# Kernel optimization log

Hardware: AMD Instinct MI355X
Metric: run time of the kernel (lower is better)

The kernel has to match this reference:

```python
import jax, jax.numpy as jnp
import numpy as np

B, N, P, D = 32, 128, 8, 512


def setup_inputs() -> dict:
    key = jax.random.key(0)
    k_x, k_w1, k_b1, k_w2, k_b2 = jax.random.split(key, 5)
    lim = 1.0 / np.sqrt(D)  # torch Linear init range
    x = jax.random.normal(k_x, (B, N, P, D), dtype=jnp.float32)
    # torch Linear weights are [out, in]; stack per-patch -> [P, D, D]
    W1 = jax.random.uniform(k_w1, (P, D, D), minval=-lim, maxval=lim, dtype=jnp.float32)
    b1 = jax.random.uniform(k_b1, (P, D), minval=-lim, maxval=lim, dtype=jnp.float32)
    W2 = jax.random.uniform(k_w2, (P, D, D), minval=-lim, maxval=lim, dtype=jnp.float32)
    b2 = jax.random.uniform(k_b2, (P, D), minval=-lim, maxval=lim, dtype=jnp.float32)
    return {"x": x, "W1": W1, "b1": b1, "W2": W2, "b2": b2}


def reference(x, W1, b1, W2, b2):
    # Per-patch 2-layer MLP with GELU, batched as one grouped GEMM pair.
    # torch Linear: y = x @ W.T + b  ->  einsum over 'kd' with W[p, k, d]
    h = jnp.einsum('bnpd,pkd->bnpk', x, W1) + b1  # [B, N, P, D]
    h = jax.nn.gelu(h, approximate=False)          # nn.GELU default is exact
    o = jnp.einsum('bnpd,pkd->bnpk', h, W2) + b2  # [B, N, P, D]
    # Dropout p=0.0 -> identity. Residual add.
    return o + x
```

## Files before the change

kernel.cpp:

```cpp
#include <hip/hip_runtime.h>
#include <stdint.h>


typedef unsigned short u16;
typedef __attribute__((ext_vector_type(8))) short bf16x8;
typedef __attribute__((ext_vector_type(4))) float f32x4;

#define AS1 __attribute__((address_space(1)))
#define AS3 __attribute__((address_space(3)))

#define MTOT 4096
#define PATCHES 8
#define DDIM 512
#define ROWSTRIDE 4096

__device__ __forceinline__ void glds16(const void* g, void* l) {
  __builtin_amdgcn_global_load_lds((const AS1 uint32_t*)g, (AS3 uint32_t*)l, 16, 0, 0);
}

__device__ __forceinline__ u16 bf16_rne(float v) {
  union { float f; uint32_t u; } c; c.f = v;
  uint32_t u = c.u + 0x7FFFu + ((c.u >> 16) & 1u);
  return (u16)(u >> 16);
}
__device__ __forceinline__ float bf16_to_f(u16 h) {
  union { uint32_t u; float f; } c; c.u = ((uint32_t)h) << 16;
  return c.f;
}
__device__ __forceinline__ void split2(float v, u16& hi, u16& lo) {
  hi = bf16_rne(v);
  float r = v - bf16_to_f(hi);
  lo = bf16_rne(r);
}

__global__ void split3_kernel(const float* __restrict__ x,  u16* xhi,  u16* xlo,  int nx,
                              const float* __restrict__ w1, u16* w1hi, u16* w1lo,
                              const float* __restrict__ w2, u16* w2hi, u16* w2lo, int nw) {
  const int total4 = (nx + 2 * nw) >> 2;
  for (int i4 = blockIdx.x * blockDim.x + threadIdx.x; i4 < total4;
       i4 += gridDim.x * blockDim.x) {
    int i = i4 << 2;
    const float* src; u16* h; u16* l; int off;
    if (i < nx)           { src = x;  h = xhi;  l = xlo;  off = i; }
    else if (i < nx + nw) { src = w1; h = w1hi; l = w1lo; off = i - nx; }
    else                  { src = w2; h = w2hi; l = w2lo; off = i - nx - nw; }
    float4 v = *reinterpret_cast<const float4*>(src + off);
    ushort4 hh, ll;
    split2(v.x, hh.x, ll.x);
    split2(v.y, hh.y, ll.y);
    split2(v.z, hh.z, ll.z);
    split2(v.w, hh.w, ll.w);
    *reinterpret_cast<ushort4*>(h + off) = hh;
    *reinterpret_cast<ushort4*>(l + off) = ll;
  }
}

template <int EPI>
__global__ __launch_bounds__(512, 2) void gemm_split8(
    const u16* __restrict__ Ahi, const u16* __restrict__ Alo,
    const u16* __restrict__ Bhi, const u16* __restrict__ Blo,
    const float* __restrict__ bias,
    const float* __restrict__ resid,
    u16* __restrict__ OutHi, u16* __restrict__ OutLo,
    float* __restrict__ OutF)
{
  const int nwg = gridDim.x;
  const int bid = blockIdx.x;
  const int swz = (bid & 7) * (nwg >> 3) + (bid >> 3);
  const int nt = swz & 1;
  const int mt = (swz >> 1) & 15;
  const int p  = swz >> 5;

  __shared__ __attribute__((aligned(16))) u16 sm[2][4][256 * 32];

  const int t    = threadIdx.x;
  const int lane = t & 63;
  const int wv   = t >> 6;
  const int wr   = wv >> 2;
  const int wc   = wv & 3;
  const int fr   = lane & 15;
  const int cS   = (lane >> 4) ^ ((fr >> 1) & 3);

  const int sr0 = t >> 2;
  const int sc  = t & 3;
  const int scS = sc ^ ((sr0 >> 1) & 3);
  const int se0 = t * 8;
  const int se1 = se0 + 4096;

  const size_t aG0 = (size_t)(mt * 256 + sr0)       * ROWSTRIDE + (size_t)p * DDIM + scS * 8;
  const size_t aG1 = (size_t)(mt * 256 + sr0 + 128) * ROWSTRIDE + (size_t)p * DDIM + scS * 8;
  const size_t bG0 = ((size_t)p * DDIM + nt * 256 + sr0)       * DDIM + scS * 8;
  const size_t bG1 = ((size_t)p * DDIM + nt * 256 + sr0 + 128) * DDIM + scS * 8;

  f32x4 acc[8][4] = {};

  glds16(Ahi + aG0, &sm[0][0][se0]); glds16(Ahi + aG1, &sm[0][0][se1]);
  glds16(Alo + aG0, &sm[0][1][se0]); glds16(Alo + aG1, &sm[0][1][se1]);
  glds16(Bhi + bG0, &sm[0][2][se0]); glds16(Bhi + bG1, &sm[0][2][se1]);
  glds16(Blo + bG0, &sm[0][3][se0]); glds16(Blo + bG1, &sm[0][3][se1]);
  asm volatile("s_waitcnt vmcnt(0)" ::: "memory");
  __builtin_amdgcn_s_barrier();

#define DS_A(pl, m) (*(const bf16x8*)&sm[cur][pl][(wr * 128 + (m) * 16 + fr) * 32 + cS * 8])
#define DS_B(pl, n) (*(const bf16x8*)&sm[cur][pl][(wc * 64  + (n) * 16 + fr) * 32 + cS * 8])
#define MFMA3(m, a_h, a_l)                                                            \
  _Pragma("unroll")                                                                   \
  for (int n = 0; n < 4; ++n) {                                                       \
    acc[m][n] = __builtin_amdgcn_mfma_f32_16x16x32_bf16(a_h, bh[n], acc[m][n], 0,0,0);\
    acc[m][n] = __builtin_amdgcn_mfma_f32_16x16x32_bf16(a_l, bh[n], acc[m][n], 0,0,0);\
    acc[m][n] = __builtin_amdgcn_mfma_f32_16x16x32_bf16(a_h, bl[n], acc[m][n], 0,0,0);\
  }

  for (int kt = 0; kt < 16; ++kt) {
    const int cur = kt & 1, nxt = cur ^ 1;
    const bool stage = (kt != 15);
    const size_t ko = (size_t)(kt + 1) * 32;

    bf16x8 bh[4], bl[4];

    {
#pragma unroll
      for (int n = 0; n < 4; ++n) { bh[n] = DS_B(2, n); bl[n] = DS_B(3, n); }
      bf16x8 a0h = DS_A(0, 0), a1h = DS_A(0, 1);
      bf16x8 a0l = DS_A(1, 0), a1l = DS_A(1, 1);
      if (stage) { glds16(Ahi + aG0 + ko, &sm[nxt][0][se0]);
                   glds16(Ahi + aG1 + ko, &sm[nxt][0][se1]); }
      __builtin_amdgcn_s_barrier();
      asm volatile("s_waitcnt lgkmcnt(0)" ::: "memory");
      __builtin_amdgcn_s_setprio(1);
      MFMA3(0, a0h, a0l)
      MFMA3(1, a1h, a1l)
      __builtin_amdgcn_s_setprio(0);
      __builtin_amdgcn_s_barrier();
    }
    {
      bf16x8 a0h = DS_A(0, 2), a1h = DS_A(0, 3);
      bf16x8 a0l = DS_A(1, 2), a1l = DS_A(1, 3);
      if (stage) { glds16(Alo + aG0 + ko, &sm[nxt][1][se0]);
                   glds16(Alo + aG1 + ko, &sm[nxt][1][se1]); }
      __builtin_amdgcn_s_barrier();
      asm volatile("s_waitcnt lgkmcnt(0)" ::: "memory");
      __builtin_amdgcn_s_setprio(1);
      MFMA3(2, a0h, a0l)
      MFMA3(3, a1h, a1l)
      __builtin_amdgcn_s_setprio(0);
      __builtin_amdgcn_s_barrier();
    }
    {
      bf16x8 a0h = DS_A(0, 4), a1h = DS_A(0, 5);
      bf16x8 a0l = DS_A(1, 4), a1l = DS_A(1, 5);
      if (stage) { glds16(Bhi + bG0 + ko, &sm[nxt][2][se0]);
                   glds16(Bhi + bG1 + ko, &sm[nxt][2][se1]); }
      __builtin_amdgcn_s_barrier();
      asm volatile("s_waitcnt lgkmcnt(0)" ::: "memory");
      __builtin_amdgcn_s_setprio(1);
      MFMA3(4, a0h, a0l)
      MFMA3(5, a1h, a1l)
      __builtin_amdgcn_s_setprio(0);
      __builtin_amdgcn_s_barrier();
    }
    {
      bf16x8 a0h = DS_A(0, 6), a1h = DS_A(0, 7);
      bf16x8 a0l = DS_A(1, 6), a1l = DS_A(1, 7);
      if (stage) { glds16(Blo + bG0 + ko, &sm[nxt][3][se0]);
                   glds16(Blo + bG1 + ko, &sm[nxt][3][se1]); }
      __builtin_amdgcn_s_barrier();
      asm volatile("s_waitcnt lgkmcnt(0)" ::: "memory");
      __builtin_amdgcn_s_setprio(1);
      MFMA3(6, a0h, a0l)
      MFMA3(7, a1h, a1l)
      __builtin_amdgcn_s_setprio(0);
      asm volatile("s_waitcnt vmcnt(0)" ::: "memory");
      __builtin_amdgcn_s_barrier();
    }
  }
#undef DS_A
#undef DS_B
#undef MFMA3

  const int rquad = (lane >> 4) * 4;
#pragma unroll
  for (int j = 0; j < 4; ++j) {
    const int col = nt * 256 + wc * 64 + j * 16 + fr;
    const float bj = bias[p * DDIM + col];
#pragma unroll
    for (int i = 0; i < 8; ++i) {
      const int row = mt * 256 + wr * 128 + i * 16 + rquad;
#pragma unroll
      for (int r = 0; r < 4; ++r) {
        const size_t idx = (size_t)(row + r) * ROWSTRIDE + (size_t)p * DDIM + col;
        float o = acc[i][j][r] + bj;
        if constexpr (EPI == 1) {
          o = 0.5f * o * (1.0f + erff(o * 0.70710678118654752f));
          u16 h_, l_;
          split2(o, h_, l_);
          OutHi[idx] = h_;
          OutLo[idx] = l_;
        } else {
          OutF[idx] = o + resid[idx];
        }
      }
    }
  }
}

extern "C" void kernel_launch(void* const* d_in, const int* in_sizes, int n_in,
                              void* d_out, int out_size, void* d_ws, size_t ws_size,
                              hipStream_t stream) {
  const float* x  = (const float*)d_in[0];
  const float* W1 = (const float*)d_in[1];
  const float* b1 = (const float*)d_in[2];
  const float* W2 = (const float*)d_in[3];
  const float* b2 = (const float*)d_in[4];
  float* out = (float*)d_out;

  const int NX = MTOT * PATCHES * DDIM;
  const int NW = PATCHES * DDIM * DDIM;

  u16* ws   = (u16*)d_ws;
  u16* xhi  = ws;
  u16* xlo  = xhi + NX;
  u16* w1hi = xlo + NX;
  u16* w1lo = w1hi + NW;
  u16* w2hi = w1lo + NW;
  u16* w2lo = w2hi + NW;
  u16* hhi  = w2lo + NW;
  u16* hlo  = hhi + NX;

  split3_kernel<<<2048, 256, 0, stream>>>(x, xhi, xlo, NX,
                                          W1, w1hi, w1lo,
                                          W2, w2hi, w2lo, NW);

  gemm_split8<1><<<256, 512, 0, stream>>>(xhi, xlo, w1hi, w1lo, b1, nullptr,
                                          hhi, hlo, nullptr);
  gemm_split8<2><<<256, 512, 0, stream>>>(hhi, hlo, w2hi, w2lo, b2, x,
                                          nullptr, nullptr, out);
}
```

Baseline: 297.4 us.

## Fuse fp32 x hi/lo split into first GEMM and restructure MFMA phases

```diff
diff --git a/kernel.cpp b/kernel.cpp
--- a/kernel.cpp
+++ b/kernel.cpp
@@ -17,6 +17,11 @@
 __device__ __forceinline__ void glds16(const void* g, void* l) {
   __builtin_amdgcn_global_load_lds((const AS1 uint32_t*)g, (AS3 uint32_t*)l, 16, 0, 0);
 }
+__device__ __forceinline__ float4 gload4(const float* p) {
+  float4 r;
+  asm volatile("global_load_dwordx4 %0, %1, off" : "=v"(r) : "v"(p) : "memory");
+  return r;
+}
 
 __device__ __forceinline__ u16 bf16_rne(float v) {
   union { float f; uint32_t u; } c; c.f = v;
@@ -33,30 +38,36 @@
   lo = bf16_rne(r);
 }
 
-__global__ void split3_kernel(const float* __restrict__ x,  u16* xhi,  u16* xlo,  int nx,
-                              const float* __restrict__ w1, u16* w1hi, u16* w1lo,
-                              const float* __restrict__ w2, u16* w2hi, u16* w2lo, int nw) {
-  const int total4 = (nx + 2 * nw) >> 2;
-  for (int i4 = blockIdx.x * blockDim.x + threadIdx.x; i4 < total4;
-       i4 += gridDim.x * blockDim.x) {
-    int i = i4 << 2;
-    const float* src; u16* h; u16* l; int off;
-    if (i < nx)           { src = x;  h = xhi;  l = xlo;  off = i; }
-    else if (i < nx + nw) { src = w1; h = w1hi; l = w1lo; off = i - nx; }
-    else                  { src = w2; h = w2hi; l = w2lo; off = i - nx - nw; }
+__device__ __forceinline__ void mfma32(const bf16x8 (&A)[8], const bf16x8 (&Bv)[4],
+                                       f32x4 (&acc)[8][4]) {
+#pragma unroll
+  for (int m = 0; m < 8; ++m)
+#pragma unroll
+    for (int n = 0; n < 4; ++n)
+      acc[m][n] = __builtin_amdgcn_mfma_f32_16x16x32_bf16(A[m], Bv[n], acc[m][n], 0, 0, 0);
+}
+
+__global__ void wsplit_kernel(const float* __restrict__ w1, u16* w1hi, u16* w1lo,
+                              const float* __restrict__ w2, u16* w2hi, u16* w2lo,
+                              int nw) {
+  int i = (blockIdx.x * blockDim.x + threadIdx.x) * 4;
+  const int stride = gridDim.x * blockDim.x * 4;
+  for (; i < nw * 2; i += stride) {
+    const float* src; u16 *h, *l; int off;
+    if (i < nw) { src = w1; h = w1hi; l = w1lo; off = i; }
+    else        { src = w2; h = w2hi; l = w2lo; off = i - nw; }
     float4 v = *reinterpret_cast<const float4*>(src + off);
     ushort4 hh, ll;
-    split2(v.x, hh.x, ll.x);
-    split2(v.y, hh.y, ll.y);
-    split2(v.z, hh.z, ll.z);
-    split2(v.w, hh.w, ll.w);
+    split2(v.x, hh.x, ll.x); split2(v.y, hh.y, ll.y);
+    split2(v.z, hh.z, ll.z); split2(v.w, hh.w, ll.w);
     *reinterpret_cast<ushort4*>(h + off) = hh;
     *reinterpret_cast<ushort4*>(l + off) = ll;
   }
 }
 
-template <int EPI>
-__global__ __launch_bounds__(512, 2) void gemm_split8(
+template <int EPI, bool AFP32>
+__global__ __launch_bounds__(512, 2) void gemm_ph(
+    const float* __restrict__ Axf,
     const u16* __restrict__ Ahi, const u16* __restrict__ Alo,
     const u16* __restrict__ Bhi, const u16* __restrict__ Blo,
     const float* __restrict__ bias,
@@ -82,101 +93,165 @@
   const int cS   = (lane >> 4) ^ ((fr >> 1) & 3);
 
   const int sr0 = t >> 2;
-  const int sc  = t & 3;
-  const int scS = sc ^ ((sr0 >> 1) & 3);
-  const int se0 = t * 8;
-  const int se1 = se0 + 4096;
-
-  const size_t aG0 = (size_t)(mt * 256 + sr0)       * ROWSTRIDE + (size_t)p * DDIM + scS * 8;
-  const size_t aG1 = (size_t)(mt * 256 + sr0 + 128) * ROWSTRIDE + (size_t)p * DDIM + scS * 8;
-  const size_t bG0 = ((size_t)p * DDIM + nt * 256 + sr0)       * DDIM + scS * 8;
-  const size_t bG1 = ((size_t)p * DDIM + nt * 256 + sr0 + 128) * DDIM + scS * 8;
+  const int scS = (t & 3) ^ ((sr0 >> 1) & 3);
+  const int se0 = t * 8, se1 = se0 + 4096;
+  const size_t bG0 = ((size_t)p * DDIM + nt * 256 + sr0) * DDIM + scS * 8;
+  const size_t bG1 = bG0 + (size_t)128 * DDIM;
+  const size_t aG0 = (size_t)(mt * 256 + sr0) * ROWSTRIDE + (size_t)p * DDIM + scS * 8;
+  const size_t aG1 = aG0 + (size_t)128 * ROWSTRIDE;
+
+  const int xr  = t >> 2;
+  const int xc  = (t & 3) * 8;
+  const int xch = (t & 3) ^ ((xr >> 1) & 3);
+  const int xo0 = xr * 32 + xch * 8;
+  const int xo1 = (xr + 128) * 32 + xch * 8;
+  const float* xbase = AFP32
+      ? (Axf + (size_t)(mt * 256 + xr) * ROWSTRIDE + (size_t)p * DDIM + xc)
+      : nullptr;
 
   f32x4 acc[8][4] = {};
-
-  glds16(Ahi + aG0, &sm[0][0][se0]); glds16(Ahi + aG1, &sm[0][0][se1]);
-  glds16(Alo + aG0, &sm[0][1][se0]); glds16(Alo + aG1, &sm[0][1][se1]);
-  glds16(Bhi + bG0, &sm[0][2][se0]); glds16(Bhi + bG1, &sm[0][2][se1]);
-  glds16(Blo + bG0, &sm[0][3][se0]); glds16(Blo + bG1, &sm[0][3][se1]);
-  asm volatile("s_waitcnt vmcnt(0)" ::: "memory");
-  __builtin_amdgcn_s_barrier();
+  bf16x8 ah[8], bh[4];
+  float4 xv0, xv1, xv2, xv3;
 
 #define DS_A(pl, m) (*(const bf16x8*)&sm[cur][pl][(wr * 128 + (m) * 16 + fr) * 32 + cS * 8])
 #define DS_B(pl, n) (*(const bf16x8*)&sm[cur][pl][(wc * 64  + (n) * 16 + fr) * 32 + cS * 8])
-#define MFMA3(m, a_h, a_l)                                                            \
-  _Pragma("unroll")                                                                   \
-  for (int n = 0; n < 4; ++n) {                                                       \
-    acc[m][n] = __builtin_amdgcn_mfma_f32_16x16x32_bf16(a_h, bh[n], acc[m][n], 0,0,0);\
-    acc[m][n] = __builtin_amdgcn_mfma_f32_16x16x32_bf16(a_l, bh[n], acc[m][n], 0,0,0);\
-    acc[m][n] = __builtin_amdgcn_mfma_f32_16x16x32_bf16(a_h, bl[n], acc[m][n], 0,0,0);\
-  }
-
-  for (int kt = 0; kt < 16; ++kt) {
+#define SPLIT_WRITE(BUF) do {                                                  \
+    union { u16 u[8]; bf16x8 v; } H0, L0, H1, L1;                              \
+    _Pragma("unroll")                                                          \
+    for (int q = 0; q < 4; ++q) {                                              \
+      split2(((const float*)&xv0)[q], H0.u[q],     L0.u[q]);                   \
+      split2(((const float*)&xv1)[q], H0.u[q + 4], L0.u[q + 4]);               \
+      split2(((const float*)&xv2)[q], H1.u[q],     L1.u[q]);                   \
+      split2(((const float*)&xv3)[q], H1.u[q + 4], L1.u[q + 4]);               \
+    }                                                                          \
+    *(bf16x8*)&sm[BUF][0][xo0] = H0.v;  *(bf16x8*)&sm[BUF][1][xo0] = L0.v;     \
+    *(bf16x8*)&sm[BUF][0][xo1] = H1.v;  *(bf16x8*)&sm[BUF][1][xo1] = L1.v;     \
+  } while (0)
+
+  if constexpr (AFP32) {
+    xv0 = gload4(xbase);
+    xv1 = gload4(xbase + 4);
+    xv2 = gload4(xbase + (size_t)128 * ROWSTRIDE);
+    xv3 = gload4(xbase + (size_t)128 * ROWSTRIDE + 4);
+    glds16(Bhi + bG0, &sm[0][2][se0]); glds16(Bhi + bG1, &sm[0][2][se1]);
+    glds16(Blo + bG0, &sm[0][3][se0]); glds16(Blo + bG1, &sm[0][3][se1]);
+    asm volatile("s_waitcnt vmcnt(0)" ::: "memory");
+    __builtin_amdgcn_sched_barrier(0);
+    SPLIT_WRITE(0);
+    asm volatile("s_waitcnt lgkmcnt(0)" ::: "memory");
+  } else {
+    glds16(Ahi + aG0, &sm[0][0][se0]); glds16(Ahi + aG1, &sm[0][0][se1]);
+    glds16(Bhi + bG0, &sm[0][2][se0]); glds16(Bhi + bG1, &sm[0][2][se1]);
+    glds16(Blo + bG0, &sm[0][3][se0]); glds16(Blo + bG1, &sm[0][3][se1]);
+    glds16(Alo + aG0, &sm[0][1][se0]); glds16(Alo + aG1, &sm[0][1][se1]);
+    asm volatile("s_waitcnt vmcnt(0)" ::: "memory");
+  }
+  __builtin_amdgcn_s_barrier();
+
+  for (int kt = 0; kt < 15; ++kt) {
     const int cur = kt & 1, nxt = cur ^ 1;
-    const bool stage = (kt != 15);
     const size_t ko = (size_t)(kt + 1) * 32;
 
-    bf16x8 bh[4], bl[4];
+#pragma unroll
+    for (int n = 0; n < 4; ++n) bh[n] = DS_B(2, n);
+#pragma unroll
+    for (int m = 0; m < 8; ++m) ah[m] = DS_A(0, m);
+    if constexpr (AFP32) {
+      xv0 = gload4(xbase + ko);
+      xv1 = gload4(xbase + ko + 4);
+      xv2 = gload4(xbase + ko + (size_t)128 * ROWSTRIDE);
+      xv3 = gload4(xbase + ko + (size_t)128 * ROWSTRIDE + 4);
+    } else {
+      glds16(Ahi + aG0 + ko, &sm[nxt][0][se0]); glds16(Ahi + aG1 + ko, &sm[nxt][0][se1]);
+    }
+    glds16(Bhi + bG0 + ko, &sm[nxt][2][se0]); glds16(Bhi + bG1 + ko, &sm[nxt][2][se1]);
+    __builtin_amdgcn_s_barrier();
+    asm volatile("s_waitcnt lgkmcnt(0)" ::: "memory");
+    __builtin_amdgcn_s_setprio(1);
+    mfma32(ah, bh, acc);
+    __builtin_amdgcn_s_setprio(0);
+    asm volatile("s_waitcnt vmcnt(6)" ::: "memory");
+    __builtin_amdgcn_s_barrier();
 
     {
-#pragma unroll
-      for (int n = 0; n < 4; ++n) { bh[n] = DS_B(2, n); bl[n] = DS_B(3, n); }
-      bf16x8 a0h = DS_A(0, 0), a1h = DS_A(0, 1);
-      bf16x8 a0l = DS_A(1, 0), a1l = DS_A(1, 1);
-      if (stage) { glds16(Ahi + aG0 + ko, &sm[nxt][0][se0]);
-                   glds16(Ahi + aG1 + ko, &sm[nxt][0][se1]); }
+      bf16x8 bl[4];
+#pragma unroll
+      for (int n = 0; n < 4; ++n) bl[n] = DS_B(3, n);
+      glds16(Blo + bG0 + ko, &sm[nxt][3][se0]); glds16(Blo + bG1 + ko, &sm[nxt][3][se1]);
       __builtin_amdgcn_s_barrier();
       asm volatile("s_waitcnt lgkmcnt(0)" ::: "memory");
       __builtin_amdgcn_s_setprio(1);
-      MFMA3(0, a0h, a0l)
-      MFMA3(1, a1h, a1l)
+      mfma32(ah, bl, acc);
       __builtin_amdgcn_s_setprio(0);
-      __builtin_amdgcn_s_barrier();
-    }
+      if constexpr (!AFP32)
+        asm volatile("s_waitcnt vmcnt(6)" ::: "memory");
+      __builtin_amdgcn_s_barrier();
+    }
+
     {
-      bf16x8 a0h = DS_A(0, 2), a1h = DS_A(0, 3);
-      bf16x8 a0l = DS_A(1, 2), a1l = DS_A(1, 3);
-      if (stage) { glds16(Alo + aG0 + ko, &sm[nxt][1][se0]);
-                   glds16(Alo + aG1 + ko, &sm[nxt][1][se1]); }
+      bf16x8 al[8];
+#pragma unroll
+      for (int m = 0; m < 8; ++m) al[m] = DS_A(1, m);
+      if constexpr (!AFP32) {
+        glds16(Alo + aG0 + ko, &sm[nxt][1][se0]); glds16(Alo + aG1 + ko, &sm[nxt][1][se1]);
+      }
       __builtin_amdgcn_s_barrier();
       asm volatile("s_waitcnt lgkmcnt(0)" ::: "memory");
       __builtin_amdgcn_s_setprio(1);
-      MFMA3(2, a0h, a0l)
-      MFMA3(3, a1h, a1l)
+      mfma32(al, bh, acc);
       __builtin_amdgcn_s_setprio(0);
-      __builtin_amdgcn_s_barrier();
-    }
+      if constexpr (AFP32) {
+        asm volatile("s_waitcnt vmcnt(4)" ::: "memory");
+        __builtin_amdgcn_sched_barrier(0);
+        SPLIT_WRITE(nxt);
+        asm volatile("s_waitcnt vmcnt(2) lgkmcnt(0)" ::: "memory");
+      } else {
+        asm volatile("s_waitcnt vmcnt(4)" ::: "memory");
+      }
+      __builtin_amdgcn_s_barrier();
+    }
+  }
+
+  {
+    const int cur = 1;
+#pragma unroll
+    for (int n = 0; n < 4; ++n) bh[n] = DS_B(2, n);
+#pragma unroll
+    for (int m = 0; m < 8; ++m) ah[m] = DS_A(0, m);
+    __builtin_amdgcn_s_barrier();
+    asm volatile("s_waitcnt lgkmcnt(0)" ::: "memory");
+    __builtin_amdgcn_s_setprio(1);
+    mfma32(ah, bh, acc);
+    __builtin_amdgcn_s_setprio(0);
+    if constexpr (AFP32) asm volatile("s_waitcnt vmcnt(0)" ::: "memory");
+    else                 asm volatile("s_waitcnt vmcnt(2)" ::: "memory");
+    __builtin_amdgcn_s_barrier();
     {
-      bf16x8 a0h = DS_A(0, 4), a1h = DS_A(0, 5);
-      bf16x8 a0l = DS_A(1, 4), a1l = DS_A(1, 5);
-      if (stage) { glds16(Bhi + bG0 + ko, &sm[nxt][2][se0]);
-                   glds16(Bhi + bG1 + ko, &sm[nxt][2][se1]); }
+      bf16x8 bl[4];
+#pragma unroll
+      for (int n = 0; n < 4; ++n) bl[n] = DS_B(3, n);
       __builtin_amdgcn_s_barrier();
       asm volatile("s_waitcnt lgkmcnt(0)" ::: "memory");
       __builtin_amdgcn_s_setprio(1);
-      MFMA3(4, a0h, a0l)
-      MFMA3(5, a1h, a1l)
+      mfma32(ah, bl, acc);
       __builtin_amdgcn_s_setprio(0);
+      if constexpr (!AFP32) asm volatile("s_waitcnt vmcnt(0)" ::: "memory");
       __builtin_amdgcn_s_barrier();
     }
     {
-      bf16x8 a0h = DS_A(0, 6), a1h = DS_A(0, 7);
-      bf16x8 a0l = DS_A(1, 6), a1l = DS_A(1, 7);
-      if (stage) { glds16(Blo + bG0 + ko, &sm[nxt][3][se0]);
-                   glds16(Blo + bG1 + ko, &sm[nxt][3][se1]); }
+      bf16x8 al[8];
+#pragma unroll
+      for (int m = 0; m < 8; ++m) al[m] = DS_A(1, m);
       __builtin_amdgcn_s_barrier();
       asm volatile("s_waitcnt lgkmcnt(0)" ::: "memory");
       __builtin_amdgcn_s_setprio(1);
-      MFMA3(6, a0h, a0l)
-      MFMA3(7, a1h, a1l)
+      mfma32(al, bh, acc);
       __builtin_amdgcn_s_setprio(0);
-      asm volatile("s_waitcnt vmcnt(0)" ::: "memory");
-      __builtin_amdgcn_s_barrier();
     }
   }
 #undef DS_A
 #undef DS_B
-#undef MFMA3
+#undef SPLIT_WRITE
 
   const int rquad = (lane >> 4) * 4;
 #pragma unroll
@@ -218,21 +293,17 @@
   const int NW = PATCHES * DDIM * DDIM;
 
   u16* ws   = (u16*)d_ws;
-  u16* xhi  = ws;
-  u16* xlo  = xhi + NX;
-  u16* w1hi = xlo + NX;
+  u16* w1hi = ws;
   u16* w1lo = w1hi + NW;
   u16* w2hi = w1lo + NW;
   u16* w2lo = w2hi + NW;
   u16* hhi  = w2lo + NW;
   u16* hlo  = hhi + NX;
 
-  split3_kernel<<<2048, 256, 0, stream>>>(x, xhi, xlo, NX,
-                                          W1, w1hi, w1lo,
-                                          W2, w2hi, w2lo, NW);
-
-  gemm_split8<1><<<256, 512, 0, stream>>>(xhi, xlo, w1hi, w1lo, b1, nullptr,
-                                          hhi, hlo, nullptr);
-  gemm_split8<2><<<256, 512, 0, stream>>>(hhi, hlo, w2hi, w2lo, b2, x,
-                                          nullptr, nullptr, out);
-}
+  wsplit_kernel<<<1024, 256, 0, stream>>>(W1, w1hi, w1lo, W2, w2hi, w2lo, NW);
+
+  gemm_ph<1, true ><<<256, 512, 0, stream>>>(x, nullptr, nullptr, w1hi, w1lo,
+                                             b1, nullptr, hhi, hlo, nullptr);
+  gemm_ph<2, false><<<256, 512, 0, stream>>>(nullptr, hhi, hlo, w2hi, w2lo,
+                                             b2, x, nullptr, nullptr, out);
+}
```

After: 261.4 us. 12.1% less time.
